# Optimization experiments

Hardware: AMD Instinct MI355X
Metric: run time of the kernel (lower is better)

The kernel has to match this reference:

```python
import jax, jax.numpy as jnp
import numpy as np

A, E, O = 8, 4096, 256          # agents, envs-per-agent, obs dim
H1, H2, H3 = 1024, 1024, 512     # idims
S = 4                            # number of shared (SEPS) networks


def setup_inputs() -> dict:
    key = jax.random.key(0)
    ks = jax.random.split(key, 8)
    f32 = jnp.float32
    return {
        "x": jax.random.normal(ks[0], (A, E, O), f32),
        "W1": jax.random.normal(ks[1], (S, O, H1), f32) * (1.0 / np.sqrt(O)),
        "b1": jnp.zeros((S, H1), f32),
        "W2": jax.random.normal(ks[2], (S, H1, H2), f32) * (np.sqrt(2.0) / np.sqrt(H1)),
        "b2": jnp.zeros((S, H2), f32),
        "W3": jax.random.normal(ks[3], (S, H2, H3), f32) * (np.sqrt(2.0) / np.sqrt(H2)),
        "b3": jnp.zeros((S, H3), f32),
        "seps_idx": jax.random.randint(ks[4], (A,), 0, S, dtype=jnp.int64),
    }


def reference(x, W1, b1, W2, b2, W3, b3, seps_idx):
    # x: [A, E, O]. Each of the S nets is applied (as in the original Python
    # loop) to the full stacked input, then the per-agent output is gathered
    # by seps_idx. MLP: Linear -> ReLU -> Linear -> ReLU -> Linear.
    def mlp(w1, bb1, w2, bb2, w3, bb3):
        h = jax.nn.relu(jnp.einsum('aeo,oh->aeh', x, w1) + bb1)
        h = jax.nn.relu(jnp.einsum('aeh,hg->aeg', h, w2) + bb2)
        return jnp.einsum('aeg,gk->aek', h, w3) + bb3

    out = jax.vmap(mlp)(W1, b1, W2, b2, W3, b3)           # [S, A, E, H3]
    sel = out[seps_idx, jnp.arange(A)]                    # [A, E, H3]
    return sel
```

## Files before the change

kernel.cpp:

```cpp
#include <hip/hip_runtime.h>
#include <hip/hip_bf16.h>


typedef unsigned short u16;
typedef __bf16 bf16x8 __attribute__((ext_vector_type(8)));
typedef float floatx4 __attribute__((ext_vector_type(4)));

__device__ __forceinline__ u16 f2bf(float f) {
    union { float f; unsigned int u; } v; v.f = f;
    unsigned int u = v.u;
    return (u16)((u + 0x7FFFu + ((u >> 16) & 1u)) >> 16);
}

__device__ __forceinline__ void load16(const void* g, void* l) {
    __builtin_amdgcn_global_load_lds(
        (const __attribute__((address_space(1))) void*)(unsigned long long)g,
        (__attribute__((address_space(3))) void*)(unsigned int)(unsigned long long)l,
        16, 0, 0);
}

__global__ __launch_bounds__(256) void prep(
    const float* __restrict__ x, u16* __restrict__ xb,
    const float* __restrict__ W1, u16* __restrict__ w1t,
    const float* __restrict__ W2, u16* __restrict__ w2t,
    const float* __restrict__ W3, u16* __restrict__ w3t) {
    __shared__ float tile[32][33];
    int b = blockIdx.x;
    const int tid = threadIdx.x;
    if (b < 8192) {
        int i = (b * 256 + tid) * 4;
        float4 v = *(const float4*)(x + i);
        ushort4 o;
        o.x = f2bf(v.x); o.y = f2bf(v.y); o.z = f2bf(v.z); o.w = f2bf(v.w);
        *(ushort4*)(xb + i) = o;
        return;
    }
    b -= 8192;
    const float* src; u16* dst; int K, N, n0, k0, s;
    if (b < 1024) {
        s = b >> 8; int r = b & 255;
        K = 256; N = 1024; n0 = (r & 31) * 32; k0 = (r >> 5) * 32;
        src = W1; dst = w1t;
    } else if (b < 5120) {
        b -= 1024; s = b >> 10; int r = b & 1023;
        K = 1024; N = 1024; n0 = (r & 31) * 32; k0 = (r >> 5) * 32;
        src = W2; dst = w2t;
    } else {
        b -= 5120; s = b >> 9; int r = b & 511;
        K = 1024; N = 512; n0 = (r & 15) * 32; k0 = (r >> 4) * 32;
        src = W3; dst = w3t;
    }
    src += (size_t)s * K * N;
    dst += (size_t)s * N * K;
    const int tx = tid & 31, ty = tid >> 5;
#pragma unroll
    for (int j = 0; j < 32; j += 8)
        tile[ty + j][tx] = src[(size_t)(k0 + ty + j) * N + (n0 + tx)];
    __syncthreads();
#pragma unroll
    for (int j = 0; j < 32; j += 8)
        dst[(size_t)(n0 + ty + j) * K + (k0 + tx)] = f2bf(tile[tx][ty + j]);
}

#define VMCNT(n) asm volatile("s_waitcnt vmcnt(" #n ")" ::: "memory")
#define SB0 __builtin_amdgcn_sched_barrier(0)

template <int K, int N, bool RELU, bool OUT_BF16>
__global__ __launch_bounds__(512, 2) void gemm_mlp(
    const u16* __restrict__ Amat, const u16* __restrict__ Wt,
    const float* __restrict__ bias, const int* __restrict__ seps,
    void* __restrict__ outp) {
    constexpr int P = K / 32;
    constexpr int NNB = N / 256;
    constexpr int LNB = (NNB == 4) ? 2 : 1;
    extern __shared__ u16 lds[];

    const int tid = threadIdx.x;
    const int wave = tid >> 6, lane = tid & 63;
    const int wm = wave >> 2, wn = wave & 3;
    const int quad = lane >> 4, l16 = lane & 15;

    const int bidx = blockIdx.x;
    const int t = bidx >> 3;
    const int mb = (t >> LNB) * 8 + (bidx & 7);
    const int nb = t & (NNB - 1);
    const int m0 = mb * 256, n0 = nb * 256;

    const int s = seps[m0 >> 12];
    const u16* Ab = Amat + (size_t)m0 * K;
    const u16* Bb = Wt + ((size_t)s * N + n0) * K;

    const int srow = (wave << 5) + (lane >> 2);
    const int gsw = (((lane & 3) ^ ((lane >> 3) & 3)) << 3);
    const u16* gA = Ab + (size_t)srow * K + gsw;
    const u16* gB = Bb + (size_t)srow * K + gsw;
    const unsigned lw = (unsigned)(wave << 10);

    auto STAGE = [&](int p) {
        u16* ub = &lds[(p & 3) << 14];
        const int kо = p << 5;
#pragma unroll
        for (int j = 0; j < 2; ++j) {
            load16(gA + (size_t)(j << 4) * K + kо, ub + lw + (j << 9));
            load16(gB + (size_t)(j << 4) * K + kо, ub + 8192 + lw + (j << 9));
        }
    };

    const int sA = (quad ^ ((l16 >> 1) & 3)) << 3;
    const int a0 = (((wm << 7) + l16) << 5) + sA;
    const int b0 = 8192 + (((wn << 6) + l16) << 5) + sA;

    floatx4 acc[8][4];
#pragma unroll
    for (int i = 0; i < 8; ++i)
#pragma unroll
        for (int j = 0; j < 4; ++j) acc[i][j] = (floatx4){0.f, 0.f, 0.f, 0.f};

    STAGE(0); STAGE(1); STAGE(2);

    bf16x8 af[8], bf[4];

#pragma unroll 1
    for (int p = 0; p < P; ++p) {
        if (p <= P - 3)      { VMCNT(8); }
        else if (p == P - 2) { VMCNT(4); }
        else                 { VMCNT(0); }
        SB0;
        __builtin_amdgcn_s_barrier();
        SB0;

        const u16* buf = &lds[(p & 3) << 14];
        if (p + 3 < P) STAGE(p + 3);
        af[0] = *(const bf16x8*)&buf[a0];
#pragma unroll
        for (int nf = 0; nf < 4; ++nf)
            bf[nf] = *(const bf16x8*)&buf[b0 + (nf << 9)];
#pragma unroll
        for (int i = 1; i < 8; ++i)
            af[i] = *(const bf16x8*)&buf[a0 + (i << 9)];

        __builtin_amdgcn_s_setprio(1);
#pragma unroll
        for (int i = 0; i < 8; ++i)
#pragma unroll
            for (int nf = 0; nf < 4; ++nf)
                acc[i][nf] = __builtin_amdgcn_mfma_f32_16x16x32_bf16(
                    af[i], bf[nf], acc[i][nf], 0, 0, 0);
        __builtin_amdgcn_s_setprio(0);
    }
    __syncthreads();

    float* eps = (float*)lds;
    constexpr int EW = 268;
    float bv[4];
#pragma unroll
    for (int nf = 0; nf < 4; ++nf)
        bv[nf] = bias[s * N + n0 + (wn << 6) + (nf << 4) + l16];

    const int rL = tid & 63;
    const int rw = tid >> 6;

#pragma unroll
    for (int mf = 0; mf < 8; ++mf) {
#pragma unroll
        for (int nf = 0; nf < 4; ++nf)
#pragma unroll
            for (int r = 0; r < 4; ++r) {
                float v = acc[mf][nf][r] + bv[nf];
                if (RELU) v = fmaxf(v, 0.0f);
                eps[((wm << 4) + (quad << 2) + r) * EW + (wn << 6) + (nf << 4) + l16] = v;
            }
        __syncthreads();
#pragma unroll
        for (int j = 0; j < 4; ++j) {
            const int er = rw + (j << 3);
            const int grow = m0 + ((er >> 4) << 7) + (mf << 4) + (er & 15);
            const float4 v = *(const float4*)&eps[er * EW + (rL << 2)];
            if (OUT_BF16) {
                ushort4 o;
                o.x = f2bf(v.x); o.y = f2bf(v.y); o.z = f2bf(v.z); o.w = f2bf(v.w);
                *(ushort4*)((u16*)outp + (size_t)grow * N + n0 + (rL << 2)) = o;
            } else {
                *(float4*)((float*)outp + (size_t)grow * N + n0 + (rL << 2)) = v;
            }
        }
        __syncthreads();
    }
}

extern "C" void kernel_launch(void* const* d_in, const int* in_sizes, int n_in,
                              void* d_out, int out_size, void* d_ws, size_t ws_size,
                              hipStream_t stream) {
    const float* x  = (const float*)d_in[0];
    const float* W1 = (const float*)d_in[1];
    const float* b1 = (const float*)d_in[2];
    const float* W2 = (const float*)d_in[3];
    const float* b2 = (const float*)d_in[4];
    const float* W3 = (const float*)d_in[5];
    const float* b3 = (const float*)d_in[6];
    const int* seps = (const int*)d_in[7];

    char* ws = (char*)d_ws;
    u16* w1t = (u16*)(ws);
    u16* w2t = (u16*)(ws + (2ull << 20));
    u16* w3t = (u16*)(ws + (10ull << 20));
    u16* xb  = (u16*)(ws + (14ull << 20));
    u16* h1  = (u16*)(ws + (30ull << 20));
    u16* h2  = (u16*)(ws + (94ull << 20));

    static int attr_once = []() {
        auto k1 = gemm_mlp<256, 1024, true, true>;
        auto k2 = gemm_mlp<1024, 1024, true, true>;
        auto k3 = gemm_mlp<1024, 512, false, false>;
        hipFuncSetAttribute(reinterpret_cast<const void*>(k1),
                            hipFuncAttributeMaxDynamicSharedMemorySize, 131072);
        hipFuncSetAttribute(reinterpret_cast<const void*>(k2),
                            hipFuncAttributeMaxDynamicSharedMemorySize, 131072);
        hipFuncSetAttribute(reinterpret_cast<const void*>(k3),
                            hipFuncAttributeMaxDynamicSharedMemorySize, 131072);
        return 0;
    }();
    (void)attr_once;

    prep<<<15360, 256, 0, stream>>>(x, xb, W1, w1t, W2, w2t, W3, w3t);

    gemm_mlp<256, 1024, true, true><<<512, 512, 131072, stream>>>(xb, w1t, b1, seps, h1);
    gemm_mlp<1024, 1024, true, true><<<512, 512, 131072, stream>>>(h1, w2t, b2, seps, h2);
    gemm_mlp<1024, 512, false, false><<<256, 512, 131072, stream>>>(h2, w3t, b3, seps, d_out);
}
```

Measured before the change: 264.5 us.

## Shrink GEMM tile to 256x128 with 3-stage pipeline for higher occupancy

Changes each GEMM block tile from 256x256 to 256x128, reorganises the waves into a 4x2 grid, and drops the LDS ring from 4 stages to 3 with smaller buffers (72KB). This permits more resident blocks per CU and launches twice as many blocks, aiming for better latency hiding and load balance. The epilogue is rewritten to stage one 64-row slab at a time and write 16 contiguous elements per thread. The trade-off is lower arithmetic intensity per block, since each A tile is reloaded for twice as many N tiles.

```diff
diff --git a/kernel.cpp b/kernel.cpp
--- a/kernel.cpp
+++ b/kernel.cpp
@@ -66,122 +66,143 @@
 #define SB0 __builtin_amdgcn_sched_barrier(0)
 
 template <int K, int N, bool RELU, bool OUT_BF16>
-__global__ __launch_bounds__(512, 2) void gemm_mlp(
+__global__ __launch_bounds__(512, 4) void gemm_mlp(
     const u16* __restrict__ Amat, const u16* __restrict__ Wt,
     const float* __restrict__ bias, const int* __restrict__ seps,
     void* __restrict__ outp) {
     constexpr int P = K / 32;
-    constexpr int NNB = N / 256;
-    constexpr int LNB = (NNB == 4) ? 2 : 1;
+    constexpr int NNB = N / 128;
+    constexpr int LNB = (NNB == 8) ? 3 : 2;
+    constexpr int UNIT = 12288;
     extern __shared__ u16 lds[];
 
     const int tid = threadIdx.x;
     const int wave = tid >> 6, lane = tid & 63;
-    const int wm = wave >> 2, wn = wave & 3;
+    const int wm = wave >> 1, wn = wave & 1;
     const int quad = lane >> 4, l16 = lane & 15;
 
     const int bidx = blockIdx.x;
     const int t = bidx >> 3;
     const int mb = (t >> LNB) * 8 + (bidx & 7);
     const int nb = t & (NNB - 1);
-    const int m0 = mb * 256, n0 = nb * 256;
+    const int m0 = mb * 256, n0 = nb * 128;
 
     const int s = seps[m0 >> 12];
     const u16* Ab = Amat + (size_t)m0 * K;
     const u16* Bb = Wt + ((size_t)s * N + n0) * K;
 
-    const int srow = (wave << 5) + (lane >> 2);
+    const int rin = lane >> 2;
     const int gsw = (((lane & 3) ^ ((lane >> 3) & 3)) << 3);
-    const u16* gA = Ab + (size_t)srow * K + gsw;
-    const u16* gB = Bb + (size_t)srow * K + gsw;
-    const unsigned lw = (unsigned)(wave << 10);
-
-    auto STAGE = [&](int p) {
-        u16* ub = &lds[(p & 3) << 14];
-        const int kо = p << 5;
-#pragma unroll
-        for (int j = 0; j < 2; ++j) {
-            load16(gA + (size_t)(j << 4) * K + kо, ub + lw + (j << 9));
-            load16(gB + (size_t)(j << 4) * K + kо, ub + 8192 + lw + (j << 9));
-        }
+    const u16* gA = Ab + (size_t)((wave << 5) + rin) * K + gsw;
+    const u16* gB = Bb + (size_t)((wave << 4) + rin) * K + gsw;
+    const unsigned dA = (unsigned)(wave << 10);
+    const unsigned dB = (unsigned)(8192 + (wave << 9));
+
+    auto STAGE = [&](int p, int sb) {
+        const int ko = p << 5;
+        u16* ub = &lds[sb];
+        load16(gA + ko, ub + dA);
+        load16(gA + (size_t)16 * K + ko, ub + dA + 512);
+        load16(gB + ko, ub + dB);
     };
 
     const int sA = (quad ^ ((l16 >> 1) & 3)) << 3;
-    const int a0 = (((wm << 7) + l16) << 5) + sA;
+    const int a0 = (((wm << 6) + l16) << 5) + sA;
     const int b0 = 8192 + (((wn << 6) + l16) << 5) + sA;
 
-    floatx4 acc[8][4];
-#pragma unroll
-    for (int i = 0; i < 8; ++i)
+    floatx4 acc[4][4];
+#pragma unroll
+    for (int i = 0; i < 4; ++i)
 #pragma unroll
         for (int j = 0; j < 4; ++j) acc[i][j] = (floatx4){0.f, 0.f, 0.f, 0.f};
 
-    STAGE(0); STAGE(1); STAGE(2);
-
-    bf16x8 af[8], bf[4];
+    STAGE(0, 0); STAGE(1, UNIT);
+    int sc = 0;
+    int ss = 2 * UNIT;
+
+    bf16x8 af[4], bf[4];
 
 #pragma unroll 1
     for (int p = 0; p < P; ++p) {
-        if (p <= P - 3)      { VMCNT(8); }
-        else if (p == P - 2) { VMCNT(4); }
-        else                 { VMCNT(0); }
+        if (p < P - 1) { VMCNT(3); } else { VMCNT(0); }
         SB0;
         __builtin_amdgcn_s_barrier();
         SB0;
 
-        const u16* buf = &lds[(p & 3) << 14];
-        if (p + 3 < P) STAGE(p + 3);
+        if (p + 2 < P) STAGE(p + 2, ss);
+        const u16* buf = &lds[sc];
         af[0] = *(const bf16x8*)&buf[a0];
 #pragma unroll
         for (int nf = 0; nf < 4; ++nf)
             bf[nf] = *(const bf16x8*)&buf[b0 + (nf << 9)];
 #pragma unroll
-        for (int i = 1; i < 8; ++i)
+        for (int i = 1; i < 4; ++i)
             af[i] = *(const bf16x8*)&buf[a0 + (i << 9)];
 
         __builtin_amdgcn_s_setprio(1);
 #pragma unroll
-        for (int i = 0; i < 8; ++i)
+        for (int i = 0; i < 4; ++i)
 #pragma unroll
             for (int nf = 0; nf < 4; ++nf)
                 acc[i][nf] = __builtin_amdgcn_mfma_f32_16x16x32_bf16(
                     af[i], bf[nf], acc[i][nf], 0, 0, 0);
         __builtin_amdgcn_s_setprio(0);
+
+        sc = (sc == 2 * UNIT) ? 0 : sc + UNIT;
+        ss = (ss == 2 * UNIT) ? 0 : ss + UNIT;
     }
     __syncthreads();
 
     float* eps = (float*)lds;
-    constexpr int EW = 268;
+    constexpr int EW = 132;
     float bv[4];
 #pragma unroll
     for (int nf = 0; nf < 4; ++nf)
         bv[nf] = bias[s * N + n0 + (wn << 6) + (nf << 4) + l16];
 
-    const int rL = tid & 63;
-    const int rw = tid >> 6;
-
-#pragma unroll
-    for (int mf = 0; mf < 8; ++mf) {
-#pragma unroll
-        for (int nf = 0; nf < 4; ++nf)
-#pragma unroll
-            for (int r = 0; r < 4; ++r) {
-                float v = acc[mf][nf][r] + bv[nf];
-                if (RELU) v = fmaxf(v, 0.0f);
-                eps[((wm << 4) + (quad << 2) + r) * EW + (wn << 6) + (nf << 4) + l16] = v;
-            }
+    const int er = tid >> 3;
+    const int cg = tid & 7;
+
+#pragma unroll
+    for (int ph = 0; ph < 4; ++ph) {
+        if (wm == ph) {
+#pragma unroll
+            for (int i = 0; i < 4; ++i)
+#pragma unroll
+                for (int nf = 0; nf < 4; ++nf)
+#pragma unroll
+                    for (int r = 0; r < 4; ++r) {
+                        float v = acc[i][nf][r] + bv[nf];
+                        if (RELU) v = fmaxf(v, 0.0f);
+                        eps[((i << 4) + (quad << 2) + r) * EW +
+                            (wn << 6) + (nf << 4) + l16] = v;
+                    }
+        }
         __syncthreads();
-#pragma unroll
-        for (int j = 0; j < 4; ++j) {
-            const int er = rw + (j << 3);
-            const int grow = m0 + ((er >> 4) << 7) + (mf << 4) + (er & 15);
-            const float4 v = *(const float4*)&eps[er * EW + (rL << 2)];
+        {
+            const int grow = m0 + (ph << 6) + er;
+            const float* src = eps + er * EW + (cg << 4);
+            float4 v0 = *(const float4*)(src);
+            float4 v1 = *(const float4*)(src + 4);
+            float4 v2 = *(const float4*)(src + 8);
+            float4 v3 = *(const float4*)(src + 12);
             if (OUT_BF16) {
-                ushort4 o;
-                o.x = f2bf(v.x); o.y = f2bf(v.y); o.z = f2bf(v.z); o.w = f2bf(v.w);
-                *(ushort4*)((u16*)outp + (size_t)grow * N + n0 + (rL << 2)) = o;
+                u16* dst = (u16*)outp + (size_t)grow * N + n0 + (cg << 4);
+                ushort4 o0, o1, o2, o3;
+                o0.x = f2bf(v0.x); o0.y = f2bf(v0.y); o0.z = f2bf(v0.z); o0.w = f2bf(v0.w);
+                o1.x = f2bf(v1.x); o1.y = f2bf(v1.y); o1.z = f2bf(v1.z); o1.w = f2bf(v1.w);
+                o2.x = f2bf(v2.x); o2.y = f2bf(v2.y); o2.z = f2bf(v2.z); o2.w = f2bf(v2.w);
+                o3.x = f2bf(v3.x); o3.y = f2bf(v3.y); o3.z = f2bf(v3.z); o3.w = f2bf(v3.w);
+                *(ushort4*)(dst) = o0;
+                *(ushort4*)(dst + 4) = o1;
+                *(ushort4*)(dst + 8) = o2;
+                *(ushort4*)(dst + 12) = o3;
             } else {
-                *(float4*)((float*)outp + (size_t)grow * N + n0 + (rL << 2)) = v;
+                float* dst = (float*)outp + (size_t)grow * N + n0 + (cg << 4);
+                *(float4*)(dst) = v0;
+                *(float4*)(dst + 4) = v1;
+                *(float4*)(dst + 8) = v2;
+                *(float4*)(dst + 12) = v3;
             }
         }
         __syncthreads();
@@ -213,18 +234,18 @@
         auto k2 = gemm_mlp<1024, 1024, true, true>;
         auto k3 = gemm_mlp<1024, 512, false, false>;
         hipFuncSetAttribute(reinterpret_cast<const void*>(k1),
-                            hipFuncAttributeMaxDynamicSharedMemorySize, 131072);
+                            hipFuncAttributeMaxDynamicSharedMemorySize, 73728);
         hipFuncSetAttribute(reinterpret_cast<const void*>(k2),
-                            hipFuncAttributeMaxDynamicSharedMemorySize, 131072);
+                            hipFuncAttributeMaxDynamicSharedMemorySize, 73728);
         hipFuncSetAttribute(reinterpret_cast<const void*>(k3),
-                            hipFuncAttributeMaxDynamicSharedMemorySize, 131072);
+                            hipFuncAttributeMaxDynamicSharedMemorySize, 73728);
         return 0;
     }();
     (void)attr_once;
 
     prep<<<15360, 256, 0, stream>>>(x, xb, W1, w1t, W2, w2t, W3, w3t);
 
-    gemm_mlp<256, 1024, true, true><<<512, 512, 131072, stream>>>(xb, w1t, b1, seps, h1);
-    gemm_mlp<1024, 1024, true, true><<<512, 512, 131072, stream>>>(h1, w2t, b2, seps, h2);
-    gemm_mlp<1024, 512, false, false><<<256, 512, 131072, stream>>>(h2, w3t, b3, seps, d_out);
-}
+    gemm_mlp<256, 1024, true, true><<<1024, 512, 73728, stream>>>(xb, w1t, b1, seps, h1);
+    gemm_mlp<1024, 1024, true, true><<<1024, 512, 73728, stream>>>(h1, w2t, b2, seps, h2);
+    gemm_mlp<1024, 512, false, false><<<512, 512, 73728, stream>>>(h2, w3t, b3, seps, d_out);
+}
```

New measurement: 285.1 us. 7.8% more time.
